# Performance work log

Hardware: AMD Instinct MI355X
Metric: run time of the kernel (lower is better)

Reference implementation:

```python
import jax, jax.numpy as jnp
import numpy as np

TOTAL = 262144
FEAT = 512
NSEG = 1024


def setup_inputs() -> dict:
    key = jax.random.key(0)
    k1, k2 = jax.random.split(key)
    batch = jax.random.normal(k1, (TOTAL, FEAT), dtype=jnp.float32)
    segment_ids = jnp.sort(jax.random.randint(k2, (TOTAL,), 0, NSEG)).astype(jnp.int32)
    return {"batch": batch, "segment_ids": segment_ids, "num_segments": NSEG}


def reference(batch, segment_ids, num_segments):
    # mode='mean', keep_shape=True: per-segment mean, broadcast back to rows.
    seg_sum = jax.ops.segment_sum(batch, segment_ids, num_segments=num_segments)
    counts = jax.ops.segment_sum(
        jnp.ones((batch.shape[0],), dtype=batch.dtype), segment_ids,
        num_segments=num_segments)
    means = seg_sum / jnp.maximum(counts, 1.0)[:, None]  # [NSEG, FEAT]
    out = jnp.take(means, segment_ids, axis=0)           # keep_shape expand
    return out
```

## Files before the change

### kernel.cpp

```cpp
#include <hip/hip_runtime.h>

#define FEAT 512
#define F4   128
#define NSEG 1024

typedef float f4_t __attribute__((ext_vector_type(4)));

__global__ void seg_bounds_kernel(const int* __restrict__ seg,
                                  int* __restrict__ starts, int total) {
    int i = blockIdx.x * blockDim.x + threadIdx.x;
    if (i >= total) return;
    int cur = seg[i];
    int prev = (i == 0) ? -1 : seg[i - 1];
    for (int s = prev + 1; s <= cur; ++s) starts[s] = i;
    if (i == total - 1) {
        for (int s = cur + 1; s <= NSEG; ++s) starts[s] = total;
    }
}

__global__ __launch_bounds__(512) void seg_mean_fused_kernel(
        const float* __restrict__ batch,
        const int* __restrict__ starts,
        float* __restrict__ out) {
    const int s      = blockIdx.x;
    const int tid    = threadIdx.x;
    const int lane_f = tid & (F4 - 1);
    const int rgrp   = tid >> 7;

    const int start = starts[s];
    const int end   = starts[s + 1];
    const int count = end - start;

    const f4_t* b4 = (const f4_t*)batch;

    f4_t a0 = (f4_t)(0.f);
    f4_t a1 = (f4_t)(0.f);

    int r = start + rgrp;
    for (; r + 28 < end; r += 32) {
        const f4_t* p = b4 + (size_t)r * F4 + lane_f;
        f4_t v0 = __builtin_nontemporal_load(p + 0 * 4 * F4);
        f4_t v1 = __builtin_nontemporal_load(p + 1 * 4 * F4);
        f4_t v2 = __builtin_nontemporal_load(p + 2 * 4 * F4);
        f4_t v3 = __builtin_nontemporal_load(p + 3 * 4 * F4);
        f4_t v4 = __builtin_nontemporal_load(p + 4 * 4 * F4);
        f4_t v5 = __builtin_nontemporal_load(p + 5 * 4 * F4);
        f4_t v6 = __builtin_nontemporal_load(p + 6 * 4 * F4);
        f4_t v7 = __builtin_nontemporal_load(p + 7 * 4 * F4);
        a0 += v0; a1 += v1;
        a0 += v2; a1 += v3;
        a0 += v4; a1 += v5;
        a0 += v6; a1 += v7;
    }
    for (; r < end; r += 4) {
        a0 += __builtin_nontemporal_load(b4 + (size_t)r * F4 + lane_f);
    }
    a0 += a1;

    __shared__ f4_t red[4][F4];
    red[rgrp][lane_f] = a0;
    __syncthreads();

    if (rgrp == 0) {
        f4_t p0 = red[0][lane_f];
        f4_t p1 = red[1][lane_f];
        f4_t p2 = red[2][lane_f];
        f4_t p3 = red[3][lane_f];
        const float inv = 1.0f / (float)(count > 0 ? count : 1);
        red[0][lane_f] = (p0 + p1 + p2 + p3) * inv;
    }
    __syncthreads();

    const f4_t mean = red[0][lane_f];
    f4_t* o4 = (f4_t*)out;

    r = start + rgrp;
    for (; r + 28 < end; r += 32) {
        f4_t* q = o4 + (size_t)r * F4 + lane_f;
        __builtin_nontemporal_store(mean, q + 0 * 4 * F4);
        __builtin_nontemporal_store(mean, q + 1 * 4 * F4);
        __builtin_nontemporal_store(mean, q + 2 * 4 * F4);
        __builtin_nontemporal_store(mean, q + 3 * 4 * F4);
        __builtin_nontemporal_store(mean, q + 4 * 4 * F4);
        __builtin_nontemporal_store(mean, q + 5 * 4 * F4);
        __builtin_nontemporal_store(mean, q + 6 * 4 * F4);
        __builtin_nontemporal_store(mean, q + 7 * 4 * F4);
    }
    for (; r < end; r += 4) {
        __builtin_nontemporal_store(mean, o4 + (size_t)r * F4 + lane_f);
    }
}

extern "C" void kernel_launch(void* const* d_in, const int* in_sizes, int n_in,
                              void* d_out, int out_size, void* d_ws, size_t ws_size,
                              hipStream_t stream) {
    const float* batch = (const float*)d_in[0];
    const int*   seg   = (const int*)d_in[1];
    float*       out   = (float*)d_out;
    const int total    = in_sizes[1];

    int* starts = (int*)d_ws;

    seg_bounds_kernel<<<(total + 255) / 256, 256, 0, stream>>>(seg, starts, total);
    seg_mean_fused_kernel<<<NSEG, 512, 0, stream>>>(batch, starts, out);
}
```

Measured before the change: 210.0 us.

## Split fused segment mean into reduce and chunked broadcast kernels

```diff
diff --git a/kernel.cpp b/kernel.cpp
--- a/kernel.cpp
+++ b/kernel.cpp
@@ -18,10 +18,10 @@
     }
 }
 
-__global__ __launch_bounds__(512) void seg_mean_fused_kernel(
+__global__ __launch_bounds__(512) void seg_mean_kernel(
         const float* __restrict__ batch,
         const int* __restrict__ starts,
-        float* __restrict__ out) {
+        float* __restrict__ means) {
     const int s      = blockIdx.x;
     const int tid    = threadIdx.x;
     const int lane_f = tid & (F4 - 1);
@@ -32,7 +32,6 @@
     const int count = end - start;
 
     const f4_t* b4 = (const f4_t*)batch;
-
     f4_t a0 = (f4_t)(0.f);
     f4_t a1 = (f4_t)(0.f);
 
@@ -67,6 +66,99 @@
         f4_t p2 = red[2][lane_f];
         f4_t p3 = red[3][lane_f];
         const float inv = 1.0f / (float)(count > 0 ? count : 1);
+        ((f4_t*)means)[(size_t)s * F4 + lane_f] = (p0 + p1 + p2 + p3) * inv;
+    }
+}
+
+__global__ __launch_bounds__(256) void broadcast_chunk_kernel(
+        const int* __restrict__ seg,
+        const int* __restrict__ starts,
+        const float* __restrict__ means,
+        float* __restrict__ out, int total) {
+    const int tid  = threadIdx.x;
+    const int lane = tid & (F4 - 1);
+    const int rg   = tid >> 7;
+    const int r0   = blockIdx.x * 256;
+    if (r0 >= total) return;
+    const int r1   = min(r0 + 256, total);
+
+    const int s0 = seg[r0];
+    const int s1 = seg[r1 - 1];
+
+    const f4_t* m4 = (const f4_t*)means;
+    f4_t* o4 = (f4_t*)out;
+
+    for (int s = s0; s <= s1; ++s) {
+        const int a = max(starts[s], r0);
+        const int b = min(starts[s + 1], r1);
+        if (a >= b) continue;
+        const f4_t mean = m4[(size_t)s * F4 + lane];
+        int r = a + rg;
+        for (; r + 14 < b; r += 16) {
+            f4_t* q = o4 + (size_t)r * F4 + lane;
+            __builtin_nontemporal_store(mean, q + 0 * 2 * F4);
+            __builtin_nontemporal_store(mean, q + 1 * 2 * F4);
+            __builtin_nontemporal_store(mean, q + 2 * 2 * F4);
+            __builtin_nontemporal_store(mean, q + 3 * 2 * F4);
+            __builtin_nontemporal_store(mean, q + 4 * 2 * F4);
+            __builtin_nontemporal_store(mean, q + 5 * 2 * F4);
+            __builtin_nontemporal_store(mean, q + 6 * 2 * F4);
+            __builtin_nontemporal_store(mean, q + 7 * 2 * F4);
+        }
+        for (; r < b; r += 2) {
+            __builtin_nontemporal_store(mean, o4 + (size_t)r * F4 + lane);
+        }
+    }
+}
+
+__global__ __launch_bounds__(512) void seg_mean_fused_kernel(
+        const float* __restrict__ batch,
+        const int* __restrict__ starts,
+        float* __restrict__ out) {
+    const int s      = blockIdx.x;
+    const int tid    = threadIdx.x;
+    const int lane_f = tid & (F4 - 1);
+    const int rgrp   = tid >> 7;
+
+    const int start = starts[s];
+    const int end   = starts[s + 1];
+    const int count = end - start;
+
+    const f4_t* b4 = (const f4_t*)batch;
+    f4_t a0 = (f4_t)(0.f);
+    f4_t a1 = (f4_t)(0.f);
+
+    int r = start + rgrp;
+    for (; r + 28 < end; r += 32) {
+        const f4_t* p = b4 + (size_t)r * F4 + lane_f;
+        f4_t v0 = __builtin_nontemporal_load(p + 0 * 4 * F4);
+        f4_t v1 = __builtin_nontemporal_load(p + 1 * 4 * F4);
+        f4_t v2 = __builtin_nontemporal_load(p + 2 * 4 * F4);
+        f4_t v3 = __builtin_nontemporal_load(p + 3 * 4 * F4);
+        f4_t v4 = __builtin_nontemporal_load(p + 4 * 4 * F4);
+        f4_t v5 = __builtin_nontemporal_load(p + 5 * 4 * F4);
+        f4_t v6 = __builtin_nontemporal_load(p + 6 * 4 * F4);
+        f4_t v7 = __builtin_nontemporal_load(p + 7 * 4 * F4);
+        a0 += v0; a1 += v1;
+        a0 += v2; a1 += v3;
+        a0 += v4; a1 += v5;
+        a0 += v6; a1 += v7;
+    }
+    for (; r < end; r += 4) {
+        a0 += __builtin_nontemporal_load(b4 + (size_t)r * F4 + lane_f);
+    }
+    a0 += a1;
+
+    __shared__ f4_t red[4][F4];
+    red[rgrp][lane_f] = a0;
+    __syncthreads();
+
+    if (rgrp == 0) {
+        f4_t p0 = red[0][lane_f];
+        f4_t p1 = red[1][lane_f];
+        f4_t p2 = red[2][lane_f];
+        f4_t p3 = red[3][lane_f];
+        const float inv = 1.0f / (float)(count > 0 ? count : 1);
         red[0][lane_f] = (p0 + p1 + p2 + p3) * inv;
     }
     __syncthreads();
@@ -99,8 +191,20 @@
     float*       out   = (float*)d_out;
     const int total    = in_sizes[1];
 
-    int* starts = (int*)d_ws;
-
-    seg_bounds_kernel<<<(total + 255) / 256, 256, 0, stream>>>(seg, starts, total);
-    seg_mean_fused_kernel<<<NSEG, 512, 0, stream>>>(batch, starts, out);
-}
+    const size_t means_bytes = (size_t)NSEG * FEAT * sizeof(float);
+    const size_t need        = means_bytes + (NSEG + 1) * sizeof(int);
+
+    if (ws_size >= need) {
+        float* means  = (float*)d_ws;
+        int*   starts = (int*)((char*)d_ws + means_bytes);
+
+        seg_bounds_kernel<<<(total + 255) / 256, 256, 0, stream>>>(seg, starts, total);
+        seg_mean_kernel<<<NSEG, 512, 0, stream>>>(batch, starts, means);
+        const int nchunks = (total + 255) / 256;
+        broadcast_chunk_kernel<<<nchunks, 256, 0, stream>>>(seg, starts, means, out, total);
+    } else {
+        int* starts = (int*)d_ws;
+        seg_bounds_kernel<<<(total + 255) / 256, 256, 0, stream>>>(seg, starts, total);
+        seg_mean_fused_kernel<<<NSEG, 512, 0, stream>>>(batch, starts, out);
+    }
+}
```

New measurement: 198.7 us. 5.4% less time.
